# Kernel tuning notes

Hardware: AMD Instinct MI355X
Metric: run time of the kernel (lower is better)

The kernel has to match this reference:

```python
import math
import jax, jax.numpy as jnp
import numpy as np

S = 2048   # padded sequence length (both src and tgt)
B = 8      # batch
D = 512    # d_embed
K = 64     # num_neighbors


def setup_inputs() -> dict:
    key = jax.random.key(0)
    ks = jax.random.split(key, 12)
    f32 = jnp.float32
    src_feats = jax.random.normal(ks[0], (S, B, D), f32)
    tgt_feats = jax.random.normal(ks[1], (S, B, D), f32)
    src_xyz = jax.random.normal(ks[2], (S, B, 3), f32)
    tgt_xyz = jax.random.normal(ks[3], (S, B, 3), f32)
    # lengths in [S - S//8, S] so every row has plenty of valid keys (>= K)
    src_lens = S - jax.random.randint(ks[4], (B,), 0, S // 8)
    tgt_lens = S - jax.random.randint(ks[5], (B,), 0, S // 8)
    scale = 1.0 / math.sqrt(D)
    Wq = jax.random.normal(ks[6], (D, D), f32) * scale
    bq = jnp.zeros((D,), f32)
    Wk = jax.random.normal(ks[7], (D, D), f32) * scale
    bk = jnp.zeros((D,), f32)
    Wc = jax.random.normal(ks[8], (1, D), f32) * scale
    bc = jnp.zeros((1,), f32)
    return dict(src_feats_padded=src_feats, tgt_feats_padded=tgt_feats,
                src_xyz_padded=src_xyz, tgt_xyz_padded=tgt_xyz,
                src_lens=src_lens, tgt_lens=tgt_lens,
                Wq=Wq, bq=bq, Wk=Wk, bk=bk, Wc=Wc, bc=bc)


def _simple_attention(query, key, value, key_padding_mask, Wq, bq, Wk, bk, num_neighbors):
    # query: (Q,B,D), key: (S,B,D), value: (S,B,E), key_padding_mask: (B,S) True=pad
    d = query.shape[-1]
    q = (query @ Wq.T + bq) / math.sqrt(d)          # (Q,B,D)
    k = key @ Wk.T + bk                              # (S,B,D)
    attn = jnp.einsum('qbd,sbd->bqs', q, k)          # (B,Q,S)
    attn = attn + jnp.where(key_padding_mask, -jnp.inf, 0.0)[:, None, :]
    if num_neighbors > 0:
        # Faithful to torch's `neighbor_mask[:, :, haha] = 0` (advanced indexing):
        # the UNION of top-k column indices over all (b,q) rows is unmasked for
        # every row; all other columns get -inf.
        idx = jax.lax.top_k(attn, num_neighbors)[1]              # (B,Q,K)
        col_mask = jnp.full((attn.shape[-1],), -jnp.inf, attn.dtype)
        col_mask = col_mask.at[idx.reshape(-1)].set(0.0)         # (S,)
        attn = attn + col_mask[None, None, :]
    attn = jax.nn.softmax(attn, axis=-1)
    return jnp.einsum('bqs,sbe->qbe', attn, value)   # (Q,B,E)


def _forward(src_feats, tgt_feats, src_xyz, tgt_xyz, src_lens, tgt_lens,
             Wq, bq, Wk, bk, Wc, bc):
    n_src, b = src_feats.shape[0], src_feats.shape[1]
    n_tgt = tgt_feats.shape[0]
    src_kpm = jnp.arange(n_src)[None, :] >= src_lens[:, None]   # (B,N_src)
    tgt_kpm = jnp.arange(n_tgt)[None, :] >= tgt_lens[:, None]   # (B,N_tgt)
    src_corr = _simple_attention(src_feats, tgt_feats, tgt_xyz, tgt_kpm,
                                 Wq, bq, Wk, bk, K)             # (N_src,B,3)
    tgt_corr = _simple_attention(tgt_feats, src_feats, src_xyz, src_kpm,
                                 Wq, bq, Wk, bk, K)             # (N_tgt,B,3)
    src_overlap = src_feats @ Wc.T + bc                          # (N_src,B,1)
    tgt_overlap = tgt_feats @ Wc.T + bc                          # (N_tgt,B,1)
    return src_corr, tgt_corr, src_overlap, tgt_overlap


def reference(src_feats_padded, tgt_feats_padded, src_xyz_padded, tgt_xyz_padded,
              src_lens, tgt_lens, Wq, bq, Wk, bk, Wc, bc):
    return _forward(src_feats_padded, tgt_feats_padded, src_xyz_padded,
                    tgt_xyz_padded, src_lens, tgt_lens, Wq, bq, Wk, bk, Wc, bc)
```

## Files before the change

kernel.cpp:

```cpp
#include <hip/hip_runtime.h>

typedef __attribute__((ext_vector_type(8))) short short8;
typedef __attribute__((ext_vector_type(4))) float f32x4;
typedef __attribute__((ext_vector_type(2))) float f32x2;

#define SEQ 2048
#define BAT 8
#define DIM 512
#define RSQRT_D 0.044194173824159216f

__device__ __forceinline__ unsigned short f2bf(float x) {
  union { float f; unsigned u; } v; v.f = x;
  unsigned r = (v.u + 0x7FFFu + ((v.u >> 16) & 1u)) >> 16;
  return (unsigned short)r;
}

__device__ __forceinline__ unsigned char f2fp8(float x) {
  return (unsigned char)(__builtin_amdgcn_cvt_pk_fp8_f32(x, x, 0, false) & 0xFF);
}

__device__ __forceinline__ void gload_lds16(const void* g, void* lds_base) {
  __builtin_amdgcn_global_load_lds(
      (const __attribute__((address_space(1))) unsigned int*)g,
      (__attribute__((address_space(3))) unsigned int*)lds_base,
      16, 0, 0);
}

__global__ __launch_bounds__(256) void k_pack(
    const float* __restrict__ src, const float* __restrict__ tgt,
    const float* __restrict__ Wc, const float* __restrict__ bc,
    const float* __restrict__ sxyz, const float* __restrict__ txyz,
    const float* __restrict__ Wq, const float* __restrict__ Wk,
    unsigned short* __restrict__ srcT, unsigned short* __restrict__ tgtT,
    float4* __restrict__ Vsrc, float4* __restrict__ Vtgt,
    unsigned short* __restrict__ Wqb, unsigned short* __restrict__ Wkb,
    float* __restrict__ out) {
  int which = blockIdx.y;
  if (blockIdx.x >= 4096) {
    int e = (blockIdx.x - 4096) * 256 + threadIdx.x;
    if (which == 0) {
      int wsel = e >> 15, j = e & 32767;
      const float* wp = (wsel ? Wk : Wq) + (size_t)j * 8;
      unsigned short* o = wsel ? Wkb : Wqb;
      float4 f0 = *(const float4*)wp, f1 = *(const float4*)(wp + 4);
      uint4 pk;
      pk.x = (unsigned)f2bf(f0.x) | ((unsigned)f2bf(f0.y) << 16);
      pk.y = (unsigned)f2bf(f0.z) | ((unsigned)f2bf(f0.w) << 16);
      pk.z = (unsigned)f2bf(f1.x) | ((unsigned)f2bf(f1.y) << 16);
      pk.w = (unsigned)f2bf(f1.z) | ((unsigned)f2bf(f1.w) << 16);
      *(uint4*)(o + (size_t)j * 8) = pk;
    } else if (e < 32768) {
      int wsel = e >> 14, id = e & 16383;
      int s = id >> 3, b = id & 7;
      const float* xyz = (wsel ? txyz : sxyz) + (size_t)id * 3;
      float4 v = make_float4(xyz[0], xyz[1], xyz[2], 0.f);
      (wsel ? Vtgt : Vsrc)[b * SEQ + s] = v;
    }
    return;
  }
  int w = threadIdx.x >> 6, lane = threadIdx.x & 63;
  int row = blockIdx.x * 4 + w;
  const float* in = (which ? tgt : src) + (size_t)row * DIM;
  unsigned short* T = which ? tgtT : srcT;
  int s = row >> 3, b = row & 7;

  const float4* in4 = (const float4*)in;
  float4 f0 = in4[lane * 2], f1 = in4[lane * 2 + 1];

  uint4 pk;
  pk.x = (unsigned)f2bf(f0.x) | ((unsigned)f2bf(f0.y) << 16);
  pk.y = (unsigned)f2bf(f0.z) | ((unsigned)f2bf(f0.w) << 16);
  pk.z = (unsigned)f2bf(f1.x) | ((unsigned)f2bf(f1.y) << 16);
  pk.w = (unsigned)f2bf(f1.z) | ((unsigned)f2bf(f1.w) << 16);
  *(uint4*)(T + ((size_t)(b * SEQ + s) * DIM + lane * 8)) = pk;

  const float4* wc4 = (const float4*)Wc;
  float4 w0 = wc4[lane * 2], w1 = wc4[lane * 2 + 1];
  float d = f0.x * w0.x + f0.y * w0.y + f0.z * w0.z + f0.w * w0.w +
            f1.x * w1.x + f1.y * w1.y + f1.z * w1.z + f1.w * w1.w;
  for (int o = 32; o; o >>= 1) d += __shfl_xor(d, o);
  if (lane == 0) {
    int base = which ? (SEQ * BAT * 6 + SEQ * BAT) : (SEQ * BAT * 6);
    out[base + row] = d + bc[0];
  }
}

__global__ __launch_bounds__(256) void k_proj(
    const unsigned short* __restrict__ srcT, const unsigned short* __restrict__ tgtT,
    const unsigned short* __restrict__ Wqb, const unsigned short* __restrict__ Wkb,
    const float* __restrict__ bq, const float* __restrict__ bk,
    unsigned char* __restrict__ Qsrc, unsigned char* __restrict__ Ktgt,
    unsigned char* __restrict__ Qtgt, unsigned char* __restrict__ Ksrc) {
  __shared__ __align__(16) char at[16384];
  __shared__ __align__(16) char bt[16384];
  int id = blockIdx.x;
  int x = id & 7, t = id >> 3;
  int m = x * 16 + (t >> 4);
  int inner = t & 15;
  int n = inner & 3, z = inner >> 2;
  bool isQ = (z == 0 || z == 2);
  const unsigned short* A = (z == 0 || z == 3) ? srcT : tgtT;
  const unsigned short* W = isQ ? Wqb : Wkb;
  const float* bias = isQ ? bq : bk;
  unsigned char* O = z == 0 ? Qsrc : z == 1 ? Ktgt : z == 2 ? Qtgt : Ksrc;

  int m0 = m * 128, n0 = n * 128;
  int tid = threadIdx.x, w = tid >> 6, lane = tid & 63;
  int ln = lane & 15, quad = lane >> 4;
  int moff = (w & 1) * 64, noff = (w >> 1) * 64;

  f32x4 acc[4][4];
  f32x4 zero = {0.f, 0.f, 0.f, 0.f};
  for (int mi = 0; mi < 4; ++mi)
    for (int ni = 0; ni < 4; ++ni) acc[mi][ni] = zero;

  for (int kb = 0; kb < DIM; kb += 64) {
    #pragma unroll
    for (int it = 0; it < 4; ++it) {
      int rbase = w * 32 + it * 8;
      int r = rbase + (lane >> 3);
      int c = (lane & 7) ^ (r & 7);
      gload_lds16(A + ((size_t)(m0 + r) * DIM + kb + c * 8), &at[rbase * 128]);
      gload_lds16(W + ((size_t)(n0 + r) * DIM + kb + c * 8), &bt[rbase * 128]);
    }
    __syncthreads();
    #pragma unroll
    for (int ks = 0; ks < 2; ++ks) {
      short8 afr[4], bfr[4];
      #pragma unroll
      for (int mi = 0; mi < 4; ++mi) {
        int r = moff + mi * 16 + ln;
        int p = (ks * 4 + quad) ^ (r & 7);
        afr[mi] = *(const short8*)(&at[r * 128 + p * 16]);
      }
      #pragma unroll
      for (int ni = 0; ni < 4; ++ni) {
        int r = noff + ni * 16 + ln;
        int p = (ks * 4 + quad) ^ (r & 7);
        bfr[ni] = *(const short8*)(&bt[r * 128 + p * 16]);
      }
      #pragma unroll
      for (int mi = 0; mi < 4; ++mi)
        #pragma unroll
        for (int ni = 0; ni < 4; ++ni)
          acc[mi][ni] = __builtin_amdgcn_mfma_f32_16x16x32_bf16(afr[mi], bfr[ni], acc[mi][ni], 0, 0, 0);
    }
    __syncthreads();
  }

  for (int ni = 0; ni < 4; ++ni) {
    int n_g = n0 + noff + ni * 16 + ln;
    float bv = bias[n_g];
    for (int mi = 0; mi < 4; ++mi) {
      int m_g = m0 + moff + mi * 16 + quad * 4;
      for (int r = 0; r < 4; ++r) {
        float v = acc[mi][ni][r] + bv;
        int row = m_g + r;
        size_t pos;
        if (isQ) pos = (size_t)row * DIM + n_g;
        else     pos = (size_t)row * DIM + ((((n_g >> 3) ^ (row & 15)) << 3) | (n_g & 7));
        O[pos] = f2fp8(v);
      }
    }
  }
}

__global__ __launch_bounds__(256) void k_attn(
    const unsigned char* __restrict__ Qsrc, const unsigned char* __restrict__ Ktgt,
    const unsigned char* __restrict__ Qtgt, const unsigned char* __restrict__ Ksrc,
    const float4* __restrict__ Vsrc, const float4* __restrict__ Vtgt,
    const int* __restrict__ src_lens, const int* __restrict__ tgt_lens,
    float4* __restrict__ part) {
  __shared__ __align__(16) char klds[32768];
  int id = blockIdx.x;
  int x = id & 7, j = id >> 3;
  int group = (j >> 7) * 8 + x;
  int dir = group >> 3, b = group & 7;
  int inner = j & 127;
  int chunk = inner >> 5, qb = inner & 31;

  const unsigned char* Q = dir ? Qtgt : Qsrc;
  const unsigned char* K = dir ? Ksrc : Ktgt;
  const float4* V = dir ? Vsrc : Vtgt;
  int len = (dir ? src_lens : tgt_lens)[b];
  int k0g = chunk * 512;
  int kend = min(len, k0g + 512);
  int nk = kend - k0g;
  int nblk = (nk + 31) >> 5;
  bool tail = (nk & 31) != 0;

  int tid = threadIdx.x, w = tid >> 6, lane = tid & 63;
  int ln = lane & 15, quad = lane >> 4;
  int q0 = qb * 64 + w * 16;

  long af[16];
  {
    const unsigned char* qrow = Q + (size_t)(b * SEQ + q0 + ln) * DIM + quad * 8;
    #pragma unroll
    for (int kk = 0; kk < 16; ++kk)
      af[kk] = *(const long*)(qrow + kk * 32);
  }

  f32x2 l2[4], Ox2[4], Oy2[4], Oz2[4];
  f32x2 z2 = {0.f, 0.f};
  #pragma unroll
  for (int r = 0; r < 4; ++r) { l2[r] = z2; Ox2[r] = z2; Oy2[r] = z2; Oz2[r] = z2; }

  const unsigned char* kchunk = K + (size_t)(b * SEQ + k0g) * DIM;

  auto stage = [&](int kb, int bs) {
    const unsigned char* kbase = kchunk + (size_t)kb * 32 * DIM;
    char* dst = &klds[bs * 16384];
    #pragma unroll
    for (int it = 0; it < 4; ++it) {
      int rp = w * 4 + it;
      gload_lds16(kbase + rp * 1024 + lane * 16, dst + rp * 1024);
    }
  };

  stage(0, 0);
  __syncthreads();

  for (int kb = 0; kb < nblk; ++kb) {
    int bs = kb & 1;
    if (kb + 1 < nblk) stage(kb + 1, bs ^ 1);
    const char* buf = &klds[bs * 16384];
    const char* krow0 = buf + ln * DIM;
    const char* krow1 = buf + (16 + ln) * DIM;

    f32x4 acc0 = {0.f, 0.f, 0.f, 0.f}, acc1 = {0.f, 0.f, 0.f, 0.f};
    #pragma unroll
    for (int kk = 0; kk < 16; ++kk) {
      int pos = (((kk * 4 + quad) ^ ln) << 3);
      long b0 = *(const long*)(krow0 + pos);
      long b1 = *(const long*)(krow1 + pos);
      acc0 = __builtin_amdgcn_mfma_f32_16x16x32_fp8_fp8(af[kk], b0, acc0, 0, 0, 0);
      acc1 = __builtin_amdgcn_mfma_f32_16x16x32_fp8_fp8(af[kk], b1, acc1, 0, 0, 0);
    }

    int lk0 = kb * 32 + ln, lk1 = lk0 + 16;
    float4 V0 = V[b * SEQ + k0g + lk0];
    float4 V1 = V[b * SEQ + k0g + lk1];
    f32x2 vxx = {V0.x, V1.x}, vyy = {V0.y, V1.y}, vzz = {V0.z, V1.z};
    if (kb + 1 < nblk || !tail) {
      #pragma unroll
      for (int r = 0; r < 4; ++r) {
        f32x2 p2;
        p2.x = __expf(acc0[r] * RSQRT_D);
        p2.y = __expf(acc1[r] * RSQRT_D);
        l2[r] += p2;
        Ox2[r] += p2 * vxx; Oy2[r] += p2 * vyy; Oz2[r] += p2 * vzz;
      }
    } else {
      bool v0 = lk0 < nk, v1 = lk1 < nk;
      #pragma unroll
      for (int r = 0; r < 4; ++r) {
        f32x2 p2;
        p2.x = v0 ? __expf(acc0[r] * RSQRT_D) : 0.f;
        p2.y = v1 ? __expf(acc1[r] * RSQRT_D) : 0.f;
        l2[r] += p2;
        Ox2[r] += p2 * vxx; Oy2[r] += p2 * vyy; Oz2[r] += p2 * vzz;
      }
    }
    __syncthreads();
  }

  #pragma unroll
  for (int r = 0; r < 4; ++r) {
    float v0 = l2[r].x + l2[r].y;
    float v1 = Ox2[r].x + Ox2[r].y;
    float v2 = Oy2[r].x + Oy2[r].y;
    float v3 = Oz2[r].x + Oz2[r].y;
    #pragma unroll
    for (int o = 1; o < 16; o <<= 1) {
      v0 += __shfl_xor(v0, o);
      v1 += __shfl_xor(v1, o);
      v2 += __shfl_xor(v2, o);
      v3 += __shfl_xor(v3, o);
    }
    if (ln == 0) {
      int q = q0 + quad * 4 + r;
      part[((size_t)(dir * BAT + b) * 4 + chunk) * SEQ + q] =
          make_float4(v0, v1, v2, v3);
    }
  }
}

__global__ __launch_bounds__(256) void k_attn_reduce(
    const float4* __restrict__ part, float* __restrict__ out) {
  int t = blockIdx.x * 256 + threadIdx.x;
  int dir = t >> 14, rem = t & 16383, b = rem >> 11, q = rem & 2047;
  size_t base = ((size_t)(dir * BAT + b) * 4) * SEQ + q;
  float4 s0 = part[base];
  float4 s1 = part[base + SEQ];
  float4 s2 = part[base + 2 * SEQ];
  float4 s3 = part[base + 3 * SEQ];
  float inv = 1.f / (s0.x + s1.x + s2.x + s3.x);
  float* ob = out + (size_t)dir * (SEQ * BAT * 3) + ((size_t)q * BAT + b) * 3;
  ob[0] = (s0.y + s1.y + s2.y + s3.y) * inv;
  ob[1] = (s0.z + s1.z + s2.z + s3.z) * inv;
  ob[2] = (s0.w + s1.w + s2.w + s3.w) * inv;
}

extern "C" void kernel_launch(void* const* d_in, const int* in_sizes, int n_in,
                              void* d_out, int out_size, void* d_ws, size_t ws_size,
                              hipStream_t stream) {
  const float* src  = (const float*)d_in[0];
  const float* tgt  = (const float*)d_in[1];
  const float* sxyz = (const float*)d_in[2];
  const float* txyz = (const float*)d_in[3];
  const int* slens  = (const int*)d_in[4];
  const int* tlens  = (const int*)d_in[5];
  const float* Wq   = (const float*)d_in[6];
  const float* bq   = (const float*)d_in[7];
  const float* Wk   = (const float*)d_in[8];
  const float* bk   = (const float*)d_in[9];
  const float* Wc   = (const float*)d_in[10];
  const float* bc   = (const float*)d_in[11];
  float* out = (float*)d_out;

  char* ws = (char*)d_ws;
  size_t off = 0;
  auto carve = [&](size_t bytes) -> char* {
    char* p = ws + off;
    off += (bytes + 255) & ~(size_t)255;
    return p;
  };
  const size_t FEAT_BF  = (size_t)BAT * SEQ * DIM * 2;
  const size_t FEAT_FP8 = (size_t)BAT * SEQ * DIM;
  unsigned short* srcT = (unsigned short*)carve(FEAT_BF);
  unsigned short* tgtT = (unsigned short*)carve(FEAT_BF);
  unsigned char* Qsrc = (unsigned char*)carve(FEAT_FP8);
  unsigned char* Ktgt = (unsigned char*)carve(FEAT_FP8);
  unsigned char* Qtgt = (unsigned char*)carve(FEAT_FP8);
  unsigned char* Ksrc = (unsigned char*)carve(FEAT_FP8);
  unsigned short* Wqb  = (unsigned short*)carve((size_t)DIM * DIM * 2);
  unsigned short* Wkb  = (unsigned short*)carve((size_t)DIM * DIM * 2);
  float4* Vsrc = (float4*)carve((size_t)BAT * SEQ * 16);
  float4* Vtgt = (float4*)carve((size_t)BAT * SEQ * 16);
  float4* part = (float4*)srcT;

  k_pack<<<dim3(4352, 2), 256, 0, stream>>>(src, tgt, Wc, bc, sxyz, txyz, Wq, Wk,
                                            srcT, tgtT, Vsrc, Vtgt, Wqb, Wkb, out);
  k_proj<<<dim3(2048), 256, 0, stream>>>(srcT, tgtT, Wqb, Wkb, bq, bk,
                                         Qsrc, Ktgt, Qtgt, Ksrc);
  k_attn<<<dim3(2048), 256, 0, stream>>>(Qsrc, Ktgt, Qtgt, Ksrc, Vsrc, Vtgt,
                                         slens, tlens, part);
  k_attn_reduce<<<dim3(128), 256, 0, stream>>>(part, out);
}
```

Baseline: 265.4 us.

## Single-buffer K tiles, stage V in LDS, drop packed-f32 accumulation

Replaces the double-buffered K staging with a single 16KB LDS buffer that is loaded and then synchronized each iteration, so the global-to-LDS load no longer overlaps the MFMA work. V coordinates for the whole 512-key chunk are preloaded into LDS as separate x/y/z arrays instead of being read from global memory each iteration. The packed two-wide float accumulators and the separate fast/tail paths are replaced by scalar accumulation with a per-key validity check. This cuts LDS use, which may allow more resident blocks, at the cost of exposed load latency and an extra barrier per block.

```diff
diff --git a/kernel.cpp b/kernel.cpp
--- a/kernel.cpp
+++ b/kernel.cpp
@@ -2,7 +2,6 @@
 
 typedef __attribute__((ext_vector_type(8))) short short8;
 typedef __attribute__((ext_vector_type(4))) float f32x4;
-typedef __attribute__((ext_vector_type(2))) float f32x2;
 
 #define SEQ 2048
 #define BAT 8
@@ -171,7 +170,8 @@
     const float4* __restrict__ Vsrc, const float4* __restrict__ Vtgt,
     const int* __restrict__ src_lens, const int* __restrict__ tgt_lens,
     float4* __restrict__ part) {
-  __shared__ __align__(16) char klds[32768];
+  __shared__ __align__(16) char klds[16384];
+  __shared__ float vx[512], vy[512], vz[512];
   int id = blockIdx.x;
   int x = id & 7, j = id >> 3;
   int group = (j >> 7) * 8 + x;
@@ -185,14 +185,17 @@
   int len = (dir ? src_lens : tgt_lens)[b];
   int k0g = chunk * 512;
   int kend = min(len, k0g + 512);
-  int nk = kend - k0g;
-  int nblk = (nk + 31) >> 5;
-  bool tail = (nk & 31) != 0;
+  int nblk = (kend - k0g + 31) >> 5;
 
   int tid = threadIdx.x, w = tid >> 6, lane = tid & 63;
   int ln = lane & 15, quad = lane >> 4;
   int q0 = qb * 64 + w * 16;
 
+  for (int i = tid; i < 512; i += 256) {
+    float4 vv = V[b * SEQ + k0g + i];
+    vx[i] = vv.x; vy[i] = vv.y; vz[i] = vv.z;
+  }
+
   long af[16];
   {
     const unsigned char* qrow = Q + (size_t)(b * SEQ + q0 + ln) * DIM + quad * 8;
@@ -201,32 +204,23 @@
       af[kk] = *(const long*)(qrow + kk * 32);
   }
 
-  f32x2 l2[4], Ox2[4], Oy2[4], Oz2[4];
-  f32x2 z2 = {0.f, 0.f};
+  float l_r[4], Ox[4], Oy[4], Oz[4];
   #pragma unroll
-  for (int r = 0; r < 4; ++r) { l2[r] = z2; Ox2[r] = z2; Oy2[r] = z2; Oz2[r] = z2; }
+  for (int r = 0; r < 4; ++r) { l_r[r] = 0.f; Ox[r] = Oy[r] = Oz[r] = 0.f; }
 
   const unsigned char* kchunk = K + (size_t)(b * SEQ + k0g) * DIM;
 
-  auto stage = [&](int kb, int bs) {
+  for (int kb = 0; kb < nblk; ++kb) {
     const unsigned char* kbase = kchunk + (size_t)kb * 32 * DIM;
-    char* dst = &klds[bs * 16384];
     #pragma unroll
     for (int it = 0; it < 4; ++it) {
       int rp = w * 4 + it;
-      gload_lds16(kbase + rp * 1024 + lane * 16, dst + rp * 1024);
-    }
-  };
-
-  stage(0, 0);
-  __syncthreads();
-
-  for (int kb = 0; kb < nblk; ++kb) {
-    int bs = kb & 1;
-    if (kb + 1 < nblk) stage(kb + 1, bs ^ 1);
-    const char* buf = &klds[bs * 16384];
-    const char* krow0 = buf + ln * DIM;
-    const char* krow1 = buf + (16 + ln) * DIM;
+      gload_lds16(kbase + rp * 1024 + lane * 16, &klds[rp * 1024]);
+    }
+    __syncthreads();
+
+    const char* krow0 = klds + ln * DIM;
+    const char* krow1 = klds + (16 + ln) * DIM;
 
     f32x4 acc0 = {0.f, 0.f, 0.f, 0.f}, acc1 = {0.f, 0.f, 0.f, 0.f};
     #pragma unroll
@@ -239,38 +233,24 @@
     }
 
     int lk0 = kb * 32 + ln, lk1 = lk0 + 16;
-    float4 V0 = V[b * SEQ + k0g + lk0];
-    float4 V1 = V[b * SEQ + k0g + lk1];
-    f32x2 vxx = {V0.x, V1.x}, vyy = {V0.y, V1.y}, vzz = {V0.z, V1.z};
-    if (kb + 1 < nblk || !tail) {
-      #pragma unroll
-      for (int r = 0; r < 4; ++r) {
-        f32x2 p2;
-        p2.x = __expf(acc0[r] * RSQRT_D);
-        p2.y = __expf(acc1[r] * RSQRT_D);
-        l2[r] += p2;
-        Ox2[r] += p2 * vxx; Oy2[r] += p2 * vyy; Oz2[r] += p2 * vzz;
-      }
-    } else {
-      bool v0 = lk0 < nk, v1 = lk1 < nk;
-      #pragma unroll
-      for (int r = 0; r < 4; ++r) {
-        f32x2 p2;
-        p2.x = v0 ? __expf(acc0[r] * RSQRT_D) : 0.f;
-        p2.y = v1 ? __expf(acc1[r] * RSQRT_D) : 0.f;
-        l2[r] += p2;
-        Ox2[r] += p2 * vxx; Oy2[r] += p2 * vyy; Oz2[r] += p2 * vzz;
-      }
+    bool v0 = (k0g + lk0) < kend, v1 = (k0g + lk1) < kend;
+    float Vx0 = vx[lk0], Vy0 = vy[lk0], Vz0 = vz[lk0];
+    float Vx1 = vx[lk1], Vy1 = vy[lk1], Vz1 = vz[lk1];
+    #pragma unroll
+    for (int r = 0; r < 4; ++r) {
+      float p0 = v0 ? __expf(acc0[r] * RSQRT_D) : 0.f;
+      float p1 = v1 ? __expf(acc1[r] * RSQRT_D) : 0.f;
+      l_r[r] += p0 + p1;
+      Ox[r] += p0 * Vx0 + p1 * Vx1;
+      Oy[r] += p0 * Vy0 + p1 * Vy1;
+      Oz[r] += p0 * Vz0 + p1 * Vz1;
     }
     __syncthreads();
   }
 
   #pragma unroll
   for (int r = 0; r < 4; ++r) {
-    float v0 = l2[r].x + l2[r].y;
-    float v1 = Ox2[r].x + Ox2[r].y;
-    float v2 = Oy2[r].x + Oy2[r].y;
-    float v3 = Oz2[r].x + Oz2[r].y;
+    float v0 = l_r[r], v1 = Ox[r], v2 = Oy[r], v3 = Oz[r];
     #pragma unroll
     for (int o = 1; o < 16; o <<= 1) {
       v0 += __shfl_xor(v0, o);
```

Result: faster. 245.5 us (-7.5%).
